# Optimization experiments

Measured on AMD Instinct MI355X. Metric: run time of the kernel, lower is better.

The kernel has to match this reference:

```python
import jax, jax.numpy as jnp
import numpy as np

N_NODES = 50000
N_EDGES = 600000
N_GRAPHS = 64
IN_D, HID, EMB = 5, 128, 64
BN_EPS = 1e-5


def setup_inputs() -> dict:
    key = jax.random.key(0)
    ks = jax.random.split(key, 16)
    x = jax.random.normal(ks[0], (N_NODES, IN_D), dtype=jnp.float32)
    src = jax.random.randint(ks[1], (N_EDGES,), 0, N_NODES, dtype=jnp.int32)
    dst = jax.random.randint(ks[2], (N_EDGES,), 0, N_NODES, dtype=jnp.int32)
    batch = jnp.sort(jax.random.randint(ks[3], (N_NODES,), 0, N_GRAPHS, dtype=jnp.int32))
    def lin(k, fi, fo):
        s = 1.0 / np.sqrt(fi)
        kw, kb = jax.random.split(k)
        return (jax.random.uniform(kw, (fi, fo), jnp.float32, -s, s),
                jax.random.uniform(kb, (fo,), jnp.float32, -s, s))
    W1, b1 = lin(ks[4], IN_D, HID)
    W2, b2 = lin(ks[5], HID, HID)
    W3, b3 = lin(ks[6], HID, HID)
    Wp, bp = lin(ks[7], HID, EMB)
    g1 = 1.0 + 0.1 * jax.random.normal(ks[8], (HID,), jnp.float32)
    g2 = 1.0 + 0.1 * jax.random.normal(ks[9], (HID,), jnp.float32)
    g3 = 1.0 + 0.1 * jax.random.normal(ks[10], (HID,), jnp.float32)
    be1 = 0.1 * jax.random.normal(ks[11], (HID,), jnp.float32)
    be2 = 0.1 * jax.random.normal(ks[12], (HID,), jnp.float32)
    be3 = 0.1 * jax.random.normal(ks[13], (HID,), jnp.float32)
    return dict(x=x, src=src, dst=dst, batch=batch,
                W1=W1, b1=b1, W2=W2, b2=b2, W3=W3, b3=b3,
                g1=g1, be1=be1, g2=g2, be2=be2, g3=g3, be3=be3,
                Wp=Wp, bp=bp)


def reference(x, src, dst, batch, W1, b1, W2, b2, W3, b3,
              g1, be1, g2, be2, g3, be3, Wp, bp):
    n = x.shape[0]
    # GCNConv with self-loops and symmetric normalization (PyG default)
    loop = jnp.arange(n, dtype=src.dtype)
    s = jnp.concatenate([src, loop])
    d = jnp.concatenate([dst, loop])
    deg = jax.ops.segment_sum(jnp.ones_like(d, dtype=x.dtype), d, num_segments=n)
    dinv = jnp.where(deg > 0, jax.lax.rsqrt(deg), 0.0)
    norm = (dinv[s] * dinv[d])[:, None]  # (E+N, 1)

    def gcn(h, W, b):
        hw = h @ W                                   # (N, HID)
        msg = hw[s] * norm                           # gather + scale
        agg = jax.ops.segment_sum(msg, d, num_segments=n)
        return agg + b

    def bn_relu(h, g, be):
        # eval-mode BatchNorm1d with running_mean=0, running_var=1
        return jax.nn.relu(h * (g * jax.lax.rsqrt(jnp.asarray(1.0 + BN_EPS, h.dtype))) + be)

    h = bn_relu(gcn(x, W1, b1), g1, be1)
    h = bn_relu(gcn(h, W2, b2), g2, be2)
    h = bn_relu(gcn(h, W3, b3), g3, be3)

    # global mean pool over graphs
    sums = jax.ops.segment_sum(h, batch, num_segments=N_GRAPHS)
    cnt = jax.ops.segment_sum(jnp.ones((n,), h.dtype), batch, num_segments=N_GRAPHS)
    pooled = sums / jnp.maximum(cnt, 1.0)[:, None]
    return pooled @ Wp + bp
```

## Files before the change

### kernel.cpp

```cpp
#include <hip/hip_runtime.h>
#include <hip/hip_fp16.h>

#define N_NODES 50000
#define N_EDGES 600000
#define N_GRAPHS 64
#define IN_D 5
#define HID 128
#define EMB 64

#define CHUNK 512
#define NCHUNK ((N_NODES + CHUNK - 1) / CHUNK)
#define NREP 16
#define NLOC 4
#define TB 16

typedef _Float16 half8 __attribute__((ext_vector_type(8)));
typedef float float4v __attribute__((ext_vector_type(4)));
typedef float floatx2 __attribute__((ext_vector_type(2)));


__global__ __launch_bounds__(256) void k_init(
        int* __restrict__ cnt, float* __restrict__ psum_rep,
        const float* __restrict__ W2, const float* __restrict__ W3,
        _Float16* __restrict__ Wt2, _Float16* __restrict__ Wt3,
        int2* __restrict__ e_pack) {
    int tid = blockIdx.x * blockDim.x + threadIdx.x;
    int nt = gridDim.x * blockDim.x;
    for (int i = tid; i < N_NODES; i += nt) cnt[i] = 0;
    for (int i = tid; i < NREP * N_GRAPHS * HID; i += nt) psum_rep[i] = 0.f;
    if (tid < 8) e_pack[N_EDGES + tid] = make_int2(0, 0);
    for (int i = tid; i < 2 * HID * HID; i += nt) {
        int rem = i & (HID * HID - 1);
        int k = rem & 127, f = rem >> 7;
        if (i < HID * HID) Wt2[rem] = (_Float16)W2[k * HID + f];
        else               Wt3[rem] = (_Float16)W3[k * HID + f];
    }
}


__global__ __launch_bounds__(256) void k_count(
        const int* __restrict__ dst, int* __restrict__ cnt) {
    int e = blockIdx.x * blockDim.x + threadIdx.x;
    if (e < N_EDGES) atomicAdd(&cnt[dst[e]], 1);
}


__global__ void k_chunksum(const int* __restrict__ cnt, int* __restrict__ csum,
                           float* __restrict__ dinv) {
    __shared__ int sh[256];
    int b = blockIdx.x, t = threadIdx.x;
    int i0 = b * CHUNK + t, i1 = i0 + 256;
    int v = 0;
    if (i0 < N_NODES) { int c = cnt[i0]; v += c; dinv[i0] = rsqrtf((float)c + 1.0f); }
    if (i1 < N_NODES) { int c = cnt[i1]; v += c; dinv[i1] = rsqrtf((float)c + 1.0f); }
    sh[t] = v; __syncthreads();
    for (int off = 128; off > 0; off >>= 1) {
        if (t < off) sh[t] += sh[t + off];
        __syncthreads();
    }
    if (t == 0) csum[b] = sh[0];
}


__global__ void k_scan(const int* __restrict__ cnt, const int* __restrict__ csum,
                       int* __restrict__ row_start) {
    __shared__ int ws[4];
    int b = blockIdx.x, t = threadIdx.x;
    int lane = t & 63, w = t >> 6;

    int pre = 0;
    for (int j = lane; j < b; j += 64) pre += csum[j];
    #pragma unroll
    for (int off = 32; off > 0; off >>= 1) pre += __shfl_down(pre, off);
    pre = __shfl(pre, 0);

    int base = b * CHUNK;
    int i0 = base + 2 * t, i1 = i0 + 1;
    int c0 = (i0 < N_NODES) ? cnt[i0] : 0;
    int c1 = (i1 < N_NODES) ? cnt[i1] : 0;
    int v = c0 + c1;
    int s = v;
    #pragma unroll
    for (int off = 1; off < 64; off <<= 1) {
        int u = __shfl_up(s, off);
        if (lane >= off) s += u;
    }
    if (lane == 63) ws[w] = s;
    __syncthreads();
    if (t == 0) {
        int r = 0;
        #pragma unroll
        for (int j = 0; j < 4; ++j) { int xx = ws[j]; ws[j] = r; r += xx; }
    }
    __syncthreads();
    int excl = s - v + ws[w] + pre;
    if (i0 < N_NODES) row_start[i0] = excl;
    if (i1 < N_NODES) row_start[i1] = excl + c0;
    if (b == 0 && t == 0) row_start[N_NODES] = N_EDGES;
}


__global__ __launch_bounds__(256) void k_scatter(
        const int* __restrict__ src, const int* __restrict__ dst,
        const float* __restrict__ dinv, const int* __restrict__ row_start,
        int* __restrict__ cnt, int2* __restrict__ e_pack) {
    int e = blockIdx.x * blockDim.x + threadIdx.x;
    if (e >= N_EDGES) return;
    int d = dst[e];
    int pos = row_start[d] + atomicSub(&cnt[d], 1) - 1;
    int s = src[e];
    e_pack[pos] = make_int2(s, __float_as_int(dinv[s]));
}


__global__ __launch_bounds__(256) void k_agg5g1(
        const float* __restrict__ x, const float* __restrict__ dinv,
        const int* __restrict__ row_start, const int2* __restrict__ e_pack,
        const float* __restrict__ W1, const float* __restrict__ b1,
        const float* __restrict__ g1, const float* __restrict__ be1,
        unsigned int* __restrict__ H8) {
    int gid = blockIdx.x * blockDim.x + threadIdx.x;
    int i = gid >> 3, k = gid & 7;
    if (i >= N_NODES) return;
    float acc = 0.f;
    if (k < IN_D) {
        int beg = row_start[i], end = row_start[i + 1];
        int e = beg;
        for (; e + 3 < end; e += 4) {
            int2 p0 = e_pack[e];
            int2 p1 = e_pack[e + 1];
            int2 p2 = e_pack[e + 2];
            int2 p3 = e_pack[e + 3];
            float x0 = x[p0.x * IN_D + k];
            float x1 = x[p1.x * IN_D + k];
            float x2 = x[p2.x * IN_D + k];
            float x3 = x[p3.x * IN_D + k];
            acc = fmaf(__int_as_float(p0.y), x0, acc);
            acc = fmaf(__int_as_float(p1.y), x1, acc);
            acc = fmaf(__int_as_float(p2.y), x2, acc);
            acc = fmaf(__int_as_float(p3.y), x3, acc);
        }
        for (; e < end; ++e) {
            int2 p = e_pack[e];
            acc = fmaf(__int_as_float(p.y), x[p.x * IN_D + k], acc);
        }
        float di = dinv[i];
        acc = di * (acc + di * x[i * IN_D + k]);
    }
    int lane = threadIdx.x & 63;
    int base = lane & ~7;
    float a0 = __shfl(acc, base + 0);
    float a1 = __shfl(acc, base + 1);
    float a2 = __shfl(acc, base + 2);
    float a3 = __shfl(acc, base + 3);
    float a4 = __shfl(acc, base + 4);
    const float rs = rsqrtf(1.0f + 1e-5f);
    int f0 = k * 16;
    float vv[16];
    #pragma unroll
    for (int u = 0; u < 8; ++u) {
        int fa = f0 + u * 2, fb = fa + 1;
        float va = b1[fa], vb = b1[fb];
        va = fmaf(a0, W1[0 * HID + fa], va); vb = fmaf(a0, W1[0 * HID + fb], vb);
        va = fmaf(a1, W1[1 * HID + fa], va); vb = fmaf(a1, W1[1 * HID + fb], vb);
        va = fmaf(a2, W1[2 * HID + fa], va); vb = fmaf(a2, W1[2 * HID + fb], vb);
        va = fmaf(a3, W1[3 * HID + fa], va); vb = fmaf(a3, W1[3 * HID + fb], vb);
        va = fmaf(a4, W1[4 * HID + fa], va); vb = fmaf(a4, W1[4 * HID + fb], vb);
        va = fmaf(va, g1[fa] * rs, be1[fa]);
        vb = fmaf(vb, g1[fb] * rs, be1[fb]);
        vv[u * 2]     = va > 0.f ? va : 0.f;
        vv[u * 2 + 1] = vb > 0.f ? vb : 0.f;
    }
    unsigned int pk[4];
    #pragma unroll
    for (int q = 0; q < 4; ++q) {
        int r = __builtin_amdgcn_cvt_pk_fp8_f32(vv[4 * q + 0], vv[4 * q + 1], 0, false);
        r = __builtin_amdgcn_cvt_pk_fp8_f32(vv[4 * q + 2], vv[4 * q + 3], r, true);
        pk[q] = (unsigned int)r;
    }
    ((uint4*)(H8 + (size_t)i * 32))[k] = make_uint4(pk[0], pk[1], pk[2], pk[3]);
}


__device__ __forceinline__ void agg_node_fp8(
        const unsigned int* __restrict__ H8, const float* __restrict__ dinv,
        const int* __restrict__ row_start, const int2* __restrict__ e_pack,
        int n, int slot8, int q8, _Float16* __restrict__ asrow) {
    float acc[16];
    #pragma unroll
    for (int j = 0; j < 16; ++j) acc[j] = 0.f;
    int beg = row_start[n], end = row_start[n + 1];
    for (int e = beg; e < end; e += 8) {
        int2 pe = e_pack[e + slot8];
        float fw = (e + slot8 < end) ? __int_as_float(pe.y) : 0.f;
        uint4 g = ((const uint4*)(H8 + (size_t)pe.x * 32))[q8];
        unsigned int gw[4] = {g.x, g.y, g.z, g.w};
        #pragma unroll
        for (int q = 0; q < 4; ++q) {
            floatx2 lo = __builtin_amdgcn_cvt_pk_f32_fp8(gw[q], false);
            floatx2 hi = __builtin_amdgcn_cvt_pk_f32_fp8(gw[q], true);
            acc[4 * q + 0] = fmaf(fw, lo[0], acc[4 * q + 0]);
            acc[4 * q + 1] = fmaf(fw, lo[1], acc[4 * q + 1]);
            acc[4 * q + 2] = fmaf(fw, hi[0], acc[4 * q + 2]);
            acc[4 * q + 3] = fmaf(fw, hi[1], acc[4 * q + 3]);
        }
    }
    #pragma unroll
    for (int j = 0; j < 16; ++j) {
        float a = acc[j];
        a += __shfl_xor(a, 8);
        a += __shfl_xor(a, 16);
        a += __shfl_xor(a, 32);
        acc[j] = a;
    }
    if (slot8 == 0) {
        float di = dinv[n];
        uint4 s = ((const uint4*)(H8 + (size_t)n * 32))[q8];
        unsigned int sw[4] = {s.x, s.y, s.z, s.w};
        float sv[16];
        #pragma unroll
        for (int q = 0; q < 4; ++q) {
            floatx2 lo = __builtin_amdgcn_cvt_pk_f32_fp8(sw[q], false);
            floatx2 hi = __builtin_amdgcn_cvt_pk_f32_fp8(sw[q], true);
            sv[4 * q + 0] = lo[0]; sv[4 * q + 1] = lo[1];
            sv[4 * q + 2] = hi[0]; sv[4 * q + 3] = hi[1];
        }
        half8 o0, o1;
        #pragma unroll
        for (int j = 0; j < 8; ++j)
            o0[j] = (_Float16)(di * fmaf(di, sv[j], acc[j]));
        #pragma unroll
        for (int j = 0; j < 8; ++j)
            o1[j] = (_Float16)(di * fmaf(di, sv[j + 8], acc[j + 8]));
        *(half8*)(asrow + q8 * 16) = o0;
        *(half8*)(asrow + q8 * 16 + 8) = o1;
    }
}


__global__ __launch_bounds__(256) void k_fuse2(
        const unsigned int* __restrict__ Hin, const float* __restrict__ dinv,
        const int* __restrict__ row_start, const int2* __restrict__ e_pack,
        const _Float16* __restrict__ Wt,
        const float* __restrict__ bb, const float* __restrict__ gg,
        const float* __restrict__ bee, unsigned char* __restrict__ out8) {
    __shared__ __align__(16) _Float16 As[TB][136];
    int t = threadIdx.x;
    int w = t >> 6, lane = t & 63;
    int slot8 = lane >> 3, q8 = lane & 7;
    int nb = blockIdx.x * TB;

    #pragma unroll 1
    for (int i = 0; i < 4; ++i)
        agg_node_fp8(Hin, dinv, row_start, e_pack, nb + w * 4 + i,
                     slot8, q8, &As[w * 4 + i][0]);
    __syncthreads();

    int quad = lane >> 4, r16 = lane & 15;
    half8 a[4];
    #pragma unroll
    for (int kb = 0; kb < 4; ++kb)
        a[kb] = *(const half8*)&As[r16][(kb * 4 + quad) * 8];
    const float rs = rsqrtf(1.0f + 1e-5f);
    #pragma unroll
    for (int fi = 0; fi < 2; ++fi) {
        int f = (w * 2 + fi) * 16 + r16;
        const half8* Brow = (const half8*)(Wt + (size_t)f * 128);
        float4v acc = {0.f, 0.f, 0.f, 0.f};
        #pragma unroll
        for (int kb = 0; kb < 4; ++kb)
            acc = __builtin_amdgcn_mfma_f32_16x16x32_f16(a[kb], Brow[kb * 4 + quad],
                                                         acc, 0, 0, 0);
        float b0 = bb[f], gf = gg[f] * rs, e0 = bee[f];
        #pragma unroll
        for (int rr = 0; rr < 4; ++rr) {
            float v = fmaf(acc[rr] + b0, gf, e0);
            v = v > 0.f ? v : 0.f;
            int p = __builtin_amdgcn_cvt_pk_fp8_f32(v, 0.f, 0, false);
            out8[(size_t)(nb + quad * 4 + rr) * 128 + f] = (unsigned char)(p & 0xff);
        }
    }
}


__global__ __launch_bounds__(256) void k_fuse3(
        const unsigned int* __restrict__ Hin, const float* __restrict__ dinv,
        const int* __restrict__ row_start, const int2* __restrict__ e_pack,
        const _Float16* __restrict__ Wt,
        const float* __restrict__ bb, const float* __restrict__ gg,
        const float* __restrict__ bee, const int* __restrict__ batch,
        float* __restrict__ psum_rep) {
    __shared__ __align__(16) _Float16 As[TB][136];
    __shared__ float sh_pool[NLOC][HID];
    int t = threadIdx.x;
    int w = t >> 6, lane = t & 63;
    int slot8 = lane >> 3, q8 = lane & 7;
    int blk = (int)blockIdx.x;
    int nb = blk * TB;

    for (int i = t; i < NLOC * HID; i += 256) ((float*)sh_pool)[i] = 0.f;

    #pragma unroll 1
    for (int i = 0; i < 4; ++i)
        agg_node_fp8(Hin, dinv, row_start, e_pack, nb + w * 4 + i,
                     slot8, q8, &As[w * 4 + i][0]);

    int quad = lane >> 4, r16 = lane & 15;
    int g0 = batch[nb];
    int gi4[4];
    #pragma unroll
    for (int rr = 0; rr < 4; ++rr) gi4[rr] = batch[nb + quad * 4 + rr];
    __syncthreads();

    half8 a[4];
    #pragma unroll
    for (int kb = 0; kb < 4; ++kb)
        a[kb] = *(const half8*)&As[r16][(kb * 4 + quad) * 8];
    float* rep = psum_rep + (size_t)(blk & (NREP - 1)) * N_GRAPHS * HID;
    const float rs = rsqrtf(1.0f + 1e-5f);
    #pragma unroll
    for (int fi = 0; fi < 2; ++fi) {
        int f = (w * 2 + fi) * 16 + r16;
        const half8* Brow = (const half8*)(Wt + (size_t)f * 128);
        float4v acc = {0.f, 0.f, 0.f, 0.f};
        #pragma unroll
        for (int kb = 0; kb < 4; ++kb)
            acc = __builtin_amdgcn_mfma_f32_16x16x32_f16(a[kb], Brow[kb * 4 + quad],
                                                         acc, 0, 0, 0);
        float b0 = bb[f], gf = gg[f] * rs, e0 = bee[f];
        float partial = 0.f;
        int cur = -1;
        #pragma unroll
        for (int rr = 0; rr < 4; ++rr) {
            float v = fmaf(acc[rr] + b0, gf, e0);
            v = v > 0.f ? v : 0.f;
            int gi = gi4[rr];
            if (gi != cur) {
                if (cur >= 0) {
                    int idx = cur - g0;
                    if (idx < NLOC) atomicAdd(&sh_pool[idx][f], partial);
                    else            atomicAdd(&rep[cur * HID + f], partial);
                }
                partial = 0.f; cur = gi;
            }
            partial += v;
        }
        if (cur >= 0) {
            int idx = cur - g0;
            if (idx < NLOC) atomicAdd(&sh_pool[idx][f], partial);
            else            atomicAdd(&rep[cur * HID + f], partial);
        }
    }
    __syncthreads();
    for (int i = t; i < NLOC * HID; i += 256) {
        int idx = i >> 7, ff = i & 127;
        float v = sh_pool[idx][ff];
        int g = g0 + idx;
        if (v != 0.f && g < N_GRAPHS) atomicAdd(&rep[g * HID + ff], v);
    }
}


__device__ __forceinline__ int lower_bound_batch(const int* __restrict__ batch, int val) {
    int lo = 0, hi = N_NODES;
    while (lo < hi) {
        int mid = (lo + hi) >> 1;
        if (batch[mid] < val) lo = mid + 1;
        else hi = mid;
    }
    return lo;
}

__global__ void k_final(const float* __restrict__ psum_rep, const int* __restrict__ batch,
                        const float* __restrict__ Wp, const float* __restrict__ bp,
                        float* __restrict__ out) {
    __shared__ float s_p[HID];
    int gi = blockIdx.x, e = threadIdx.x;
    for (int f = e; f < HID; f += EMB) {
        float v = 0.f;
        #pragma unroll
        for (int r = 0; r < NREP; ++r)
            v += psum_rep[(size_t)r * N_GRAPHS * HID + gi * HID + f];
        s_p[f] = v;
    }
    int lane = e & 63;
    int r = 0;
    if (lane < 2) r = lower_bound_batch(batch, gi + lane);
    int c0 = __shfl(r, 0), c1 = __shfl(r, 1);
    float inv = 1.0f / fmaxf((float)(c1 - c0), 1.0f);
    __syncthreads();
    float acc = bp[e];
    #pragma unroll 8
    for (int f = 0; f < HID; ++f)
        acc = fmaf(s_p[f] * inv, Wp[f * EMB + e], acc);
    out[gi * EMB + e] = acc;
}


extern "C" void kernel_launch(void* const* d_in, const int* in_sizes, int n_in,
                              void* d_out, int out_size, void* d_ws, size_t ws_size,
                              hipStream_t stream) {
    const float* x   = (const float*)d_in[0];
    const int*   src = (const int*)d_in[1];
    const int*   dst = (const int*)d_in[2];
    const int* batch = (const int*)d_in[3];
    const float* W1 = (const float*)d_in[4];
    const float* b1 = (const float*)d_in[5];
    const float* W2 = (const float*)d_in[6];
    const float* b2 = (const float*)d_in[7];
    const float* W3 = (const float*)d_in[8];
    const float* b3 = (const float*)d_in[9];
    const float* g1 = (const float*)d_in[10];
    const float* be1 = (const float*)d_in[11];
    const float* g2 = (const float*)d_in[12];
    const float* be2 = (const float*)d_in[13];
    const float* g3 = (const float*)d_in[14];
    const float* be3 = (const float*)d_in[15];
    const float* Wp = (const float*)d_in[16];
    const float* bp = (const float*)d_in[17];
    float* out = (float*)d_out;

    char* ws = (char*)d_ws;
    size_t o = 0;
    auto alloc = [&](size_t bytes) {
        void* pp = ws + o;
        o += bytes;
        o = (o + 255) & ~255ull;
        return pp;
    };
    int*      cnt       = (int*)alloc(N_NODES * 4);
    int*      row_start = (int*)alloc((N_NODES + 1) * 4);
    int*      csum      = (int*)alloc(NCHUNK * 4);
    float*    dinv      = (float*)alloc(N_NODES * 4);
    int2*     e_pack    = (int2*)alloc((size_t)(N_EDGES + 8) * 8);
    _Float16* Wt2       = (_Float16*)alloc(HID * HID * 2);
    _Float16* Wt3       = (_Float16*)alloc(HID * HID * 2);
    unsigned int* H8a   = (unsigned int*)alloc((size_t)N_NODES * HID);
    unsigned int* H8b   = (unsigned int*)alloc((size_t)N_NODES * HID);
    float*    psum_rep  = (float*)alloc((size_t)NREP * N_GRAPHS * HID * 4);

    k_init<<<512, 256, 0, stream>>>(cnt, psum_rep, W2, W3, Wt2, Wt3, e_pack);
    k_count<<<(N_EDGES + 255) / 256, 256, 0, stream>>>(dst, cnt);
    k_chunksum<<<NCHUNK, 256, 0, stream>>>(cnt, csum, dinv);
    k_scan<<<NCHUNK, 256, 0, stream>>>(cnt, csum, row_start);
    k_scatter<<<(N_EDGES + 255) / 256, 256, 0, stream>>>(src, dst, dinv, row_start,
                                                         cnt, e_pack);
    k_agg5g1<<<(N_NODES * 8 + 255) / 256, 256, 0, stream>>>(x, dinv, row_start, e_pack,
                                                            W1, b1, g1, be1, H8a);
    k_fuse2<<<N_NODES / TB, 256, 0, stream>>>(H8a, dinv, row_start, e_pack, Wt2,
                                              b2, g2, be2, (unsigned char*)H8b);
    k_fuse3<<<N_NODES / TB, 256, 0, stream>>>(H8b, dinv, row_start, e_pack, Wt3,
                                              b3, g3, be3, batch, psum_rep);
    k_final<<<N_GRAPHS, EMB, 0, stream>>>(psum_rep, batch, Wp, bp, out);
}
```

Before: 276.9 us.

## Stage block edge lists in LDS and restructure layer-1 aggregation per wavefront

The 16-node block's contiguous edge range is loaded into shared memory once, and the layer-2 and layer-3 aggregations read edge entries from there, with a fallback to global memory past ECAP. Layer 1 is rewritten to the same wave-per-node scheme: x is padded to 8 floats per node in k_init, each edge slot gathers one padded feature, and the 5x128 projection uses weights held in registers. This is meant to cut uncoalesced x gathers and repeated global e_pack reads. In exchange it adds shared-memory staging, an extra barrier, and a padding pass over x.

Measured after the change: 270.6 us. -2.3%, faster.

```diff
diff --git a/kernel.cpp b/kernel.cpp
--- a/kernel.cpp
+++ b/kernel.cpp
@@ -13,6 +13,7 @@
 #define NREP 16
 #define NLOC 4
 #define TB 16
+#define ECAP 1024
 
 typedef _Float16 half8 __attribute__((ext_vector_type(8)));
 typedef float float4v __attribute__((ext_vector_type(4)));
@@ -23,12 +24,17 @@
         int* __restrict__ cnt, float* __restrict__ psum_rep,
         const float* __restrict__ W2, const float* __restrict__ W3,
         _Float16* __restrict__ Wt2, _Float16* __restrict__ Wt3,
-        int2* __restrict__ e_pack) {
+        int2* __restrict__ e_pack,
+        const float* __restrict__ x, float* __restrict__ xp) {
     int tid = blockIdx.x * blockDim.x + threadIdx.x;
     int nt = gridDim.x * blockDim.x;
     for (int i = tid; i < N_NODES; i += nt) cnt[i] = 0;
     for (int i = tid; i < NREP * N_GRAPHS * HID; i += nt) psum_rep[i] = 0.f;
     if (tid < 8) e_pack[N_EDGES + tid] = make_int2(0, 0);
+    for (int i = tid; i < N_NODES * 8; i += nt) {
+        int f = i & 7, n = i >> 3;
+        xp[i] = (f < IN_D) ? x[n * IN_D + f] : 0.f;
+    }
     for (int i = tid; i < 2 * HID * HID; i += nt) {
         int rem = i & (HID * HID - 1);
         int k = rem & 127, f = rem >> 7;
@@ -113,85 +119,86 @@
 }
 
 
-__global__ __launch_bounds__(256) void k_agg5g1(
-        const float* __restrict__ x, const float* __restrict__ dinv,
+__global__ __launch_bounds__(256) void k_agg1(
+        const float* __restrict__ xp, const float* __restrict__ dinv,
         const int* __restrict__ row_start, const int2* __restrict__ e_pack,
         const float* __restrict__ W1, const float* __restrict__ b1,
         const float* __restrict__ g1, const float* __restrict__ be1,
-        unsigned int* __restrict__ H8) {
-    int gid = blockIdx.x * blockDim.x + threadIdx.x;
-    int i = gid >> 3, k = gid & 7;
-    if (i >= N_NODES) return;
-    float acc = 0.f;
-    if (k < IN_D) {
-        int beg = row_start[i], end = row_start[i + 1];
-        int e = beg;
-        for (; e + 3 < end; e += 4) {
-            int2 p0 = e_pack[e];
-            int2 p1 = e_pack[e + 1];
-            int2 p2 = e_pack[e + 2];
-            int2 p3 = e_pack[e + 3];
-            float x0 = x[p0.x * IN_D + k];
-            float x1 = x[p1.x * IN_D + k];
-            float x2 = x[p2.x * IN_D + k];
-            float x3 = x[p3.x * IN_D + k];
-            acc = fmaf(__int_as_float(p0.y), x0, acc);
-            acc = fmaf(__int_as_float(p1.y), x1, acc);
-            acc = fmaf(__int_as_float(p2.y), x2, acc);
-            acc = fmaf(__int_as_float(p3.y), x3, acc);
-        }
-        for (; e < end; ++e) {
-            int2 p = e_pack[e];
-            acc = fmaf(__int_as_float(p.y), x[p.x * IN_D + k], acc);
-        }
-        float di = dinv[i];
-        acc = di * (acc + di * x[i * IN_D + k]);
-    }
-    int lane = threadIdx.x & 63;
-    int base = lane & ~7;
-    float a0 = __shfl(acc, base + 0);
-    float a1 = __shfl(acc, base + 1);
-    float a2 = __shfl(acc, base + 2);
-    float a3 = __shfl(acc, base + 3);
-    float a4 = __shfl(acc, base + 4);
+        unsigned short* __restrict__ H8u) {
+    __shared__ int2 eL[ECAP];
+    int t = threadIdx.x;
+    int w = t >> 6, lane = t & 63;
+    int slot8 = lane >> 3, q8 = lane & 7;
+    int nb = blockIdx.x * TB;
+
+    int E0 = row_start[nb], E1 = row_start[nb + TB];
+    int cntL = E1 - E0 + 8; if (cntL > ECAP) cntL = ECAP;
+    for (int i = t; i < cntL; i += 256) eL[i] = e_pack[E0 + i];
+    __syncthreads();
+
     const float rs = rsqrtf(1.0f + 1e-5f);
-    int f0 = k * 16;
-    float vv[16];
-    #pragma unroll
-    for (int u = 0; u < 8; ++u) {
-        int fa = f0 + u * 2, fb = fa + 1;
-        float va = b1[fa], vb = b1[fb];
-        va = fmaf(a0, W1[0 * HID + fa], va); vb = fmaf(a0, W1[0 * HID + fb], vb);
-        va = fmaf(a1, W1[1 * HID + fa], va); vb = fmaf(a1, W1[1 * HID + fb], vb);
-        va = fmaf(a2, W1[2 * HID + fa], va); vb = fmaf(a2, W1[2 * HID + fb], vb);
-        va = fmaf(a3, W1[3 * HID + fa], va); vb = fmaf(a3, W1[3 * HID + fb], vb);
-        va = fmaf(a4, W1[4 * HID + fa], va); vb = fmaf(a4, W1[4 * HID + fb], vb);
-        va = fmaf(va, g1[fa] * rs, be1[fa]);
-        vb = fmaf(vb, g1[fb] * rs, be1[fb]);
-        vv[u * 2]     = va > 0.f ? va : 0.f;
-        vv[u * 2 + 1] = vb > 0.f ? vb : 0.f;
-    }
-    unsigned int pk[4];
-    #pragma unroll
-    for (int q = 0; q < 4; ++q) {
-        int r = __builtin_amdgcn_cvt_pk_fp8_f32(vv[4 * q + 0], vv[4 * q + 1], 0, false);
-        r = __builtin_amdgcn_cvt_pk_fp8_f32(vv[4 * q + 2], vv[4 * q + 3], r, true);
-        pk[q] = (unsigned int)r;
-    }
-    ((uint4*)(H8 + (size_t)i * 32))[k] = make_uint4(pk[0], pk[1], pk[2], pk[3]);
+    int fa = lane * 2, fb = fa + 1;
+    float w1a[IN_D], w1b[IN_D];
+    #pragma unroll
+    for (int k = 0; k < IN_D; ++k) {
+        w1a[k] = W1[k * HID + fa];
+        w1b[k] = W1[k * HID + fb];
+    }
+    float b1a = b1[fa], b1b = b1[fb];
+    float g1a = g1[fa] * rs, g1b = g1[fb] * rs;
+    float e1a = be1[fa], e1b = be1[fb];
+
+    #pragma unroll 1
+    for (int i = 0; i < 4; ++i) {
+        int n = nb + w * 4 + i;
+        int beg = row_start[n], end = row_start[n + 1];
+        float acc = 0.f;
+        for (int e = beg; e < end; e += 8) {
+            int eo = e + slot8 - E0;
+            int2 pe;
+            if (eo < cntL) pe = eL[eo];
+            else           pe = e_pack[e + slot8];
+            float fw = (e + slot8 < end) ? __int_as_float(pe.y) : 0.f;
+            float g = xp[(size_t)pe.x * 8 + q8];
+            acc = fmaf(fw, g, acc);
+        }
+        acc += __shfl_xor(acc, 8);
+        acc += __shfl_xor(acc, 16);
+        acc += __shfl_xor(acc, 32);
+        float di = dinv[n];
+        float av = di * fmaf(di, xp[(size_t)n * 8 + q8], acc);
+        float a0 = __shfl(av, 0), a1 = __shfl(av, 1), a2 = __shfl(av, 2),
+              a3 = __shfl(av, 3), a4 = __shfl(av, 4);
+        float va = b1a, vb = b1b;
+        va = fmaf(a0, w1a[0], va); vb = fmaf(a0, w1b[0], vb);
+        va = fmaf(a1, w1a[1], va); vb = fmaf(a1, w1b[1], vb);
+        va = fmaf(a2, w1a[2], va); vb = fmaf(a2, w1b[2], vb);
+        va = fmaf(a3, w1a[3], va); vb = fmaf(a3, w1b[3], vb);
+        va = fmaf(a4, w1a[4], va); vb = fmaf(a4, w1b[4], vb);
+        va = fmaf(va, g1a, e1a);
+        vb = fmaf(vb, g1b, e1b);
+        va = va > 0.f ? va : 0.f;
+        vb = vb > 0.f ? vb : 0.f;
+        int p = __builtin_amdgcn_cvt_pk_fp8_f32(va, vb, 0, false);
+        H8u[(size_t)n * 64 + lane] = (unsigned short)(p & 0xffff);
+    }
 }
 
 
 __device__ __forceinline__ void agg_node_fp8(
         const unsigned int* __restrict__ H8, const float* __restrict__ dinv,
         const int* __restrict__ row_start, const int2* __restrict__ e_pack,
+        const int2* __restrict__ eL, int E0, int cntL,
         int n, int slot8, int q8, _Float16* __restrict__ asrow) {
     float acc[16];
     #pragma unroll
     for (int j = 0; j < 16; ++j) acc[j] = 0.f;
     int beg = row_start[n], end = row_start[n + 1];
     for (int e = beg; e < end; e += 8) {
-        int2 pe = e_pack[e + slot8];
+        int eo = e + slot8 - E0;
+        int2 pe;
+        if (eo < cntL) pe = eL[eo];
+        else           pe = e_pack[e + slot8];
         float fw = (e + slot8 < end) ? __int_as_float(pe.y) : 0.f;
         uint4 g = ((const uint4*)(H8 + (size_t)pe.x * 32))[q8];
         unsigned int gw[4] = {g.x, g.y, g.z, g.w};
@@ -245,15 +252,21 @@
         const float* __restrict__ bb, const float* __restrict__ gg,
         const float* __restrict__ bee, unsigned char* __restrict__ out8) {
     __shared__ __align__(16) _Float16 As[TB][136];
+    __shared__ int2 eL[ECAP];
     int t = threadIdx.x;
     int w = t >> 6, lane = t & 63;
     int slot8 = lane >> 3, q8 = lane & 7;
     int nb = blockIdx.x * TB;
 
+    int E0 = row_start[nb], E1 = row_start[nb + TB];
+    int cntL = E1 - E0 + 8; if (cntL > ECAP) cntL = ECAP;
+    for (int i = t; i < cntL; i += 256) eL[i] = e_pack[E0 + i];
+    __syncthreads();
+
     #pragma unroll 1
     for (int i = 0; i < 4; ++i)
-        agg_node_fp8(Hin, dinv, row_start, e_pack, nb + w * 4 + i,
-                     slot8, q8, &As[w * 4 + i][0]);
+        agg_node_fp8(Hin, dinv, row_start, e_pack, eL, E0, cntL,
+                     nb + w * 4 + i, slot8, q8, &As[w * 4 + i][0]);
     __syncthreads();
 
     int quad = lane >> 4, r16 = lane & 15;
@@ -291,6 +304,7 @@
         const float* __restrict__ bee, const int* __restrict__ batch,
         float* __restrict__ psum_rep) {
     __shared__ __align__(16) _Float16 As[TB][136];
+    __shared__ int2 eL[ECAP];
     __shared__ float sh_pool[NLOC][HID];
     int t = threadIdx.x;
     int w = t >> 6, lane = t & 63;
@@ -299,11 +313,15 @@
     int nb = blk * TB;
 
     for (int i = t; i < NLOC * HID; i += 256) ((float*)sh_pool)[i] = 0.f;
+    int E0 = row_start[nb], E1 = row_start[nb + TB];
+    int cntL = E1 - E0 + 8; if (cntL > ECAP) cntL = ECAP;
+    for (int i = t; i < cntL; i += 256) eL[i] = e_pack[E0 + i];
+    __syncthreads();
 
     #pragma unroll 1
     for (int i = 0; i < 4; ++i)
-        agg_node_fp8(Hin, dinv, row_start, e_pack, nb + w * 4 + i,
-                     slot8, q8, &As[w * 4 + i][0]);
+        agg_node_fp8(Hin, dinv, row_start, e_pack, eL, E0, cntL,
+                     nb + w * 4 + i, slot8, q8, &As[w * 4 + i][0]);
 
     int quad = lane >> 4, r16 = lane & 15;
     int g0 = batch[nb];
@@ -435,18 +453,19 @@
     int2*     e_pack    = (int2*)alloc((size_t)(N_EDGES + 8) * 8);
     _Float16* Wt2       = (_Float16*)alloc(HID * HID * 2);
     _Float16* Wt3       = (_Float16*)alloc(HID * HID * 2);
+    float*    xp        = (float*)alloc((size_t)N_NODES * 8 * 4);
     unsigned int* H8a   = (unsigned int*)alloc((size_t)N_NODES * HID);
     unsigned int* H8b   = (unsigned int*)alloc((size_t)N_NODES * HID);
     float*    psum_rep  = (float*)alloc((size_t)NREP * N_GRAPHS * HID * 4);
 
-    k_init<<<512, 256, 0, stream>>>(cnt, psum_rep, W2, W3, Wt2, Wt3, e_pack);
+    k_init<<<512, 256, 0, stream>>>(cnt, psum_rep, W2, W3, Wt2, Wt3, e_pack, x, xp);
     k_count<<<(N_EDGES + 255) / 256, 256, 0, stream>>>(dst, cnt);
     k_chunksum<<<NCHUNK, 256, 0, stream>>>(cnt, csum, dinv);
     k_scan<<<NCHUNK, 256, 0, stream>>>(cnt, csum, row_start);
     k_scatter<<<(N_EDGES + 255) / 256, 256, 0, stream>>>(src, dst, dinv, row_start,
                                                          cnt, e_pack);
-    k_agg5g1<<<(N_NODES * 8 + 255) / 256, 256, 0, stream>>>(x, dinv, row_start, e_pack,
-                                                            W1, b1, g1, be1, H8a);
+    k_agg1<<<N_NODES / TB, 256, 0, stream>>>(xp, dinv, row_start, e_pack,
+                                             W1, b1, g1, be1, (unsigned short*)H8a);
     k_fuse2<<<N_NODES / TB, 256, 0, stream>>>(H8a, dinv, row_start, e_pack, Wt2,
                                               b2, g2, be2, (unsigned char*)H8b);
     k_fuse3<<<N_NODES / TB, 256, 0, stream>>>(H8b, dinv, row_start, e_pack, Wt3,
```
